# Performance work log

Measured on AMD Instinct MI355X. Metric: run time of the kernel, lower is better.

Reference implementation:

```python
import jax, jax.numpy as jnp
import numpy as np

LN_EPS = 1e-5
ALPHA_Q = 1.0

def _ln(t, g, b):
    mu = jnp.mean(t, -1, keepdims=True)
    var = jnp.var(t, -1, keepdims=True)
    return (t - mu) / jnp.sqrt(var + LN_EPS) * g + b

def _mlp(t, w1, b1, w2, b2):
    h = jax.nn.gelu(t @ w1.T + b1, approximate=False)
    return h @ w2.T + b2

def setup_inputs() -> dict:
    key = jax.random.key(0)
    B, N, L, E, H, D = 2, 2048, 2048, 1024, 16, 4
    ks = jax.random.split(key, 40)
    rn = lambda i, shape, sc: jax.random.normal(ks[i], shape, jnp.float32) * sc
    inp = {}
    inp['x'] = rn(0, (B, N, E), 1.0)
    inp['xp'] = jax.random.uniform(ks[1], (B, N, D), jnp.float32)
    inp['y'] = rn(2, (B, L, E), 1.0)
    inp['yp'] = jax.random.uniform(ks[3], (B, L, D), jnp.float32)
    inp['attn_mask'] = jax.random.uniform(ks[4], (1, 1, N, L), jnp.float32)
    # PositionEncoder params (torch Linear convention: weight [out,in])
    inp['p_w1'] = rn(5, (E, D), 1.0 / D)
    inp['p_b1'] = jax.random.uniform(ks[6], (E,), jnp.float32, 0.0, np.pi)
    inp['p_w2'] = rn(7, (E, D), 1.0 / D)
    inp['p_b2'] = jax.random.uniform(ks[8], (E,), jnp.float32, 0.0, np.pi)
    # QueryEncoder: LayerNorm + mlp1 + mlp2 (mlp0 is dead code in the source)
    inp['q_ln_g'] = jnp.ones((E,), jnp.float32); inp['q_ln_b'] = jnp.zeros((E,), jnp.float32)
    inp['q_m1_w1'] = rn(9, (2 * E, E), 0.02); inp['q_m1_b1'] = jnp.zeros((2 * E,), jnp.float32)
    inp['q_m1_w2'] = rn(10, (E, 2 * E), 0.02); inp['q_m1_b2'] = jnp.zeros((E,), jnp.float32)
    inp['q_m2_w1'] = rn(11, (2 * E, E), 0.02); inp['q_m2_b1'] = jnp.zeros((2 * E,), jnp.float32)
    inp['q_m2_w2'] = rn(12, (E, 2 * E), 0.02); inp['q_m2_b2'] = jnp.zeros((E,), jnp.float32)
    # KeyEncoder: LayerNorm + mlp1 (mlp0 dead code)
    inp['k_ln_g'] = jnp.ones((E,), jnp.float32); inp['k_ln_b'] = jnp.zeros((E,), jnp.float32)
    inp['k_m1_w1'] = rn(13, (2 * E, E), 0.02); inp['k_m1_b1'] = jnp.zeros((2 * E,), jnp.float32)
    inp['k_m1_w2'] = rn(14, (E, 2 * E), 0.02); inp['k_m1_b2'] = jnp.zeros((E,), jnp.float32)
    # V: LayerNorm + Linear
    inp['v_ln_g'] = jnp.ones((E,), jnp.float32); inp['v_ln_b'] = jnp.zeros((E,), jnp.float32)
    inp['v_w'] = rn(15, (E, E), 0.02); inp['v_b'] = jnp.zeros((E,), jnp.float32)
    # output projections
    inp['proj1_w'] = rn(16, (E, E), 0.02); inp['proj1_b'] = jnp.zeros((E,), jnp.float32)
    inp['proj2_w'] = rn(17, (E, D * H), 0.02); inp['proj2_b'] = jnp.zeros((E,), jnp.float32)
    return inp

def reference(x, xp, y, yp, attn_mask, p_w1, p_b1, p_w2, p_b2,
              q_ln_g, q_ln_b, q_m1_w1, q_m1_b1, q_m1_w2, q_m1_b2,
              q_m2_w1, q_m2_b1, q_m2_w2, q_m2_b2,
              k_ln_g, k_ln_b, k_m1_w1, k_m1_b1, k_m1_w2, k_m1_b2,
              v_ln_g, v_ln_b, v_w, v_b, proj1_w, proj1_b, proj2_w, proj2_b):
    B, N, E = x.shape
    L = y.shape[1]
    D = xp.shape[2]
    H = proj2_w.shape[1] // D
    C = E // H
    # PositionEncoder: query side with bias, key side without bias
    pxt = ALPHA_Q * xp
    xp1 = pxt @ p_w1.T + p_b1            # [B,N,E]
    xp2 = pxt @ p_w2.T + p_b2
    pyt = ALPHA_Q * yp
    yp1 = pyt @ p_w1.T                   # [B,L,E], no bias
    yp2 = pyt @ p_w2.T
    rh = lambda t: t.reshape(t.shape[0], -1, H, C)
    # QueryEncoder
    xn = _ln(x, q_ln_g, q_ln_b)
    x1 = _mlp(xn, q_m1_w1, q_m1_b1, q_m1_w2, q_m1_b2)
    x2 = _mlp(xn, q_m2_w1, q_m2_b1, q_m2_w2, q_m2_b2)
    q = jnp.concatenate([rh(x1 * jnp.cos(xp1)), rh(x1 * jnp.sin(xp1)),
                         rh(x2 * jnp.cos(xp2)), rh(x2 * jnp.sin(xp2))], axis=-1)  # [B,N,H,4C]
    # KeyEncoder (note: second cos/sin block is the raw position code)
    yn = _ln(y, k_ln_g, k_ln_b)
    y1 = _mlp(yn, k_m1_w1, k_m1_b1, k_m1_w2, k_m1_b2)
    k = jnp.concatenate([rh(y1 * jnp.cos(yp1)), rh(y1 * jnp.sin(yp1)),
                         rh(jnp.cos(yp2)), rh(jnp.sin(yp2))], axis=-1)            # [B,L,H,4C]
    scale = (4 * C) ** (-0.5)
    attn = jax.nn.softmax(jnp.einsum('bnhd,blhd->bhnl', q, k) * scale, axis=-1)
    # masked renormalization (mask applied AFTER softmax)
    eps = min(1e-8, 1.0 / L)
    attn = attn * attn_mask
    attn = attn / (jnp.sum(attn, axis=-1, keepdims=True) + eps)
    # values
    v = (_ln(y, v_ln_g, v_ln_b) @ v_w.T + v_b).reshape(B, L, H, C)
    out1 = jnp.einsum('bhnl,blhc->bnhc', attn, v).reshape(B, N, E) @ proj1_w.T + proj1_b
    out2 = jnp.einsum('bhnl,bld->bnhd', attn, yp) - xp[:, :, None, :]             # [B,N,H,D]
    out2 = out2.reshape(B, N, H * D) @ proj2_w.T + proj2_b
    return (out1 + out2, attn, xp)
```

## Files before the change

kernel.cpp:

```cpp
#include <hip/hip_runtime.h>
#include <math.h>
#include <stdint.h>

#define DEV static __device__ __forceinline__

typedef __bf16 bf16x8 __attribute__((ext_vector_type(8)));
typedef __bf16 bf16x4v __attribute__((ext_vector_type(4)));
typedef float f32x4 __attribute__((ext_vector_type(4)));

constexpr int Nn = 2048, Ll = 2048, Ee = 1024, Hh = 16;
constexpr float SCALE = 0.0625f;

constexpr size_t OFF_XN   = 0;
constexpr size_t OFF_YNK  = 8388608;
constexpr size_t OFF_YNV  = 16777216;
constexpr size_t OFF_H12  = 25165824;
constexpr size_t OFF_H3   = 58720256;
constexpr size_t OFF_X1   = 75497472;
constexpr size_t OFF_X2   = 83886080;
constexpr size_t OFF_Y1   = 92274688;
constexpr size_t OFF_QWS  = 100663296;
constexpr size_t OFF_KWS  = 134217728;
constexpr size_t OFF_VWS  = 167772160;
constexpr size_t OFF_DNV  = 176160768;
constexpr size_t OFF_YPT  = 176422912;
constexpr size_t OFF_MSK  = 176685056;
constexpr size_t OFF_AVZ  = 185073664;
constexpr size_t OFF_W1122= 193986560;
constexpr size_t OFF_W12  = 202375168;
constexpr size_t OFF_W22  = 206569472;
constexpr size_t OFF_WK1  = 210763776;
constexpr size_t OFF_WK2  = 214958080;
constexpr size_t OFF_WV   = 219152384;
constexpr size_t OFF_WP   = 221249536;
constexpr size_t OFF_EM   = 223477760;

DEV void gl2l(const void* g, void* l) {
  __builtin_amdgcn_global_load_lds((const __attribute__((address_space(1))) void*)g,
                                   (__attribute__((address_space(3))) void*)l, 16, 0, 0);
}

DEV float gelu_f(float v) {
  float x = v * 0.70710678118654752f;
  float ax = fabsf(x);
  float t = 1.f / fmaf(0.3275911f, ax, 1.f);
  float y = t * fmaf(t, fmaf(t, fmaf(t, fmaf(t, 1.061405429f, -1.453152027f),
                                     1.421413741f), -0.284496736f), 0.254829592f);
  float er = 1.f - y * __expf(-x * x);
  er = (x < 0.f) ? -er : er;
  return 0.5f * v * (1.f + er);
}

__launch_bounds__(256)
__global__ void prep_ln(const float* __restrict__ s0, const float* __restrict__ s1,
                        const float* __restrict__ s2, const float* __restrict__ s3,
                        const float* __restrict__ s4, const float* __restrict__ s5,
                        const float* __restrict__ s6,
                        __bf16* __restrict__ d0, __bf16* __restrict__ d1,
                        __bf16* __restrict__ d2, __bf16* __restrict__ d3,
                        __bf16* __restrict__ d4, __bf16* __restrict__ d5,
                        __bf16* __restrict__ d6,
                        const float* __restrict__ pw1, const float* __restrict__ pw2,
                        __bf16* __restrict__ wp,
                        const float* __restrict__ mask, __bf16* __restrict__ mb,
                        const float* __restrict__ yp, __bf16* __restrict__ ypT,
                        const float* __restrict__ x, const float* __restrict__ y,
                        const float* __restrict__ qg, const float* __restrict__ qb,
                        const float* __restrict__ kg, const float* __restrict__ kb,
                        const float* __restrict__ vg, const float* __restrict__ vb,
                        __bf16* __restrict__ xn, __bf16* __restrict__ ynk,
                        __bf16* __restrict__ ynv) {
  const int tid = threadIdx.x;
  if (blockIdx.x >= 18512) {
    const int t = blockIdx.x - 18512;
    const bool isx = t < 4096;
    const int row = isx ? t : t - 4096;
    const float* src = (isx ? x : y) + (size_t)row * Ee;
    const float4 v = ((const float4*)src)[tid];
    float s = v.x + v.y + v.z + v.w;
    float q = v.x*v.x + v.y*v.y + v.z*v.z + v.w*v.w;
    #pragma unroll
    for (int o = 32; o > 0; o >>= 1) { s += __shfl_down(s, o); q += __shfl_down(q, o); }
    __shared__ float ls[4], lq[4];
    if ((tid & 63) == 0) { ls[tid >> 6] = s; lq[tid >> 6] = q; }
    __syncthreads();
    s = ls[0] + ls[1] + ls[2] + ls[3];
    q = lq[0] + lq[1] + lq[2] + lq[3];
    const float mu = s * (1.f / Ee);
    const float rstd = rsqrtf(q * (1.f / Ee) - mu * mu + 1e-5f);
    const int e0 = tid << 2;
    float h0 = (v.x - mu) * rstd, h1 = (v.y - mu) * rstd,
          h2 = (v.z - mu) * rstd, h3 = (v.w - mu) * rstd;
    if (isx) {
      bf16x4v o;
      o[0] = (__bf16)(h0 * qg[e0]   + qb[e0]);
      o[1] = (__bf16)(h1 * qg[e0+1] + qb[e0+1]);
      o[2] = (__bf16)(h2 * qg[e0+2] + qb[e0+2]);
      o[3] = (__bf16)(h3 * qg[e0+3] + qb[e0+3]);
      *(bf16x4v*)(xn + (size_t)row * Ee + e0) = o;
    } else {
      bf16x4v ok, ov;
      ok[0] = (__bf16)(h0 * kg[e0]   + kb[e0]);
      ok[1] = (__bf16)(h1 * kg[e0+1] + kb[e0+1]);
      ok[2] = (__bf16)(h2 * kg[e0+2] + kb[e0+2]);
      ok[3] = (__bf16)(h3 * kg[e0+3] + kb[e0+3]);
      ov[0] = (__bf16)(h0 * vg[e0]   + vb[e0]);
      ov[1] = (__bf16)(h1 * vg[e0+1] + vb[e0+1]);
      ov[2] = (__bf16)(h2 * vg[e0+2] + vb[e0+2]);
      ov[3] = (__bf16)(h3 * vg[e0+3] + vb[e0+3]);
      *(bf16x4v*)(ynk + (size_t)row * Ee + e0) = ok;
      *(bf16x4v*)(ynv + (size_t)row * Ee + e0) = ov;
    }
    return;
  }
  int u = blockIdx.x * 256 + tid;
  if (u < 3407872) {
    int seg = u >> 19, r = u & 524287;
    const float* s; __bf16* d;
    if      (seg == 0) { s = s0; d = d0; }
    else if (seg == 1) { s = s1; d = d1; }
    else if (seg == 2) { s = s2; d = d2; }
    else if (seg == 3) { s = s3; d = d3; }
    else if (seg == 4) { s = s4; d = d4; }
    else if (seg == 5) { s = s5; d = d5; }
    else               { s = s6; d = d6; }
    float4 v = ((const float4*)s)[r];
    bf16x4v o; o[0]=(__bf16)v.x; o[1]=(__bf16)v.y; o[2]=(__bf16)v.z; o[3]=(__bf16)v.w;
    ((bf16x4v*)d)[r] = o;
  } else if (u < 3686400) {
    int p = u - 3407872;
    int row = p / 272, c4 = p - row * 272;
    float4 v = (c4 < 256) ? ((const float4*)pw1)[row * 256 + c4]
                          : ((const float4*)pw2)[row * 16 + (c4 - 256)];
    bf16x4v o; o[0]=(__bf16)v.x; o[1]=(__bf16)v.y; o[2]=(__bf16)v.z; o[3]=(__bf16)v.w;
    *(bf16x4v*)(wp + (size_t)row * 1088 + (c4 << 2)) = o;
  } else if (u < 4734976) {
    int q = u - 3686400;
    float4 v = ((const float4*)mask)[q];
    bf16x4v o; o[0]=(__bf16)v.x; o[1]=(__bf16)v.y; o[2]=(__bf16)v.z; o[3]=(__bf16)v.w;
    ((bf16x4v*)mb)[q] = o;
  } else {
    int t0 = (u - 4734976) << 2;
    #pragma unroll
    for (int k = 0; k < 4; k++) {
      int i = t0 + k;
      int b = i >> 13, d = (i >> 11) & 3, l = i & 2047;
      ypT[i] = (__bf16)yp[(((size_t)b << 11) + l) * 4 + d];
    }
  }
}

#define STAGE_A(BM_, A_, lda_, kt_, kh_, buf_)                                        \
  _Pragma("unroll")                                                                   \
  for (int jj = 0; jj < (BM_) / 128; jj++) {                                          \
    int c = (jj << 9) + tid;                                                          \
    int row_ = c >> 2, j_ = c & 3;                                                    \
    int col_ = ((kt_) << 6) + ((kh_) << 5) + ((j_ ^ (row_ & 3)) << 3);                \
    gl2l(A_ + (size_t)(m0 + row_) * (lda_) + col_,                                    \
         As + ((((buf_) << 1) + (kh_)) * ((BM_) * 32)) + (c << 3));                   \
  }

#define STAGE_B(W_, ldw_, kt_, kh_, buf_)                                             \
  _Pragma("unroll")                                                                   \
  for (int jj = 0; jj < 2; jj++) {                                                    \
    int c = (jj << 9) + tid;                                                          \
    int row_ = c >> 2, j_ = c & 3;                                                    \
    int col_ = ((kt_) << 6) + ((kh_) << 5) + ((j_ ^ (row_ & 3)) << 3);                \
    gl2l(W_ + (size_t)(n0 + row_) * (ldw_) + col_,                                    \
         Bs + ((((buf_) << 1) + (kh_)) * 8192) + (c << 3));                           \
  }

#define LOAD_A(BM_, buf_, ks_)                                                        \
  _Pragma("unroll")                                                                   \
  for (int i = 0; i < (BM_) / 32; i++) {                                              \
    int ra = wm + (i << 4) + li;                                                      \
    af[i] = *(const bf16x8*)(As + ((((buf_) << 1) + (ks_)) * ((BM_) * 32))            \
             + ra * 32 + ((g ^ (ra & 3)) << 3));                                      \
  }

#define LOAD_B(buf_, ks_, qn_)                                                        \
  _Pragma("unroll")                                                                   \
  for (int jj = 0; jj < 2; jj++) {                                                    \
    int rb = wn + ((qn_) << 5) + (jj << 4) + li;                                      \
    bw[jj] = *(const bf16x8*)(Bs + ((((buf_) << 1) + (ks_)) * 8192)                   \
             + rb * 32 + ((g ^ (rb & 3)) << 3));                                      \
  }

#define MFMA_Q(BM_, qn_)                                                              \
  __builtin_amdgcn_s_setprio(1);                                                      \
  _Pragma("unroll")                                                                   \
  for (int i = 0; i < (BM_) / 32; i++) {                                              \
    acc[i][((qn_) << 1)]     = __builtin_amdgcn_mfma_f32_16x16x32_bf16(af[i], bw[0], acc[i][((qn_) << 1)], 0, 0, 0);     \
    acc[i][((qn_) << 1) + 1] = __builtin_amdgcn_mfma_f32_16x16x32_bf16(af[i], bw[1], acc[i][((qn_) << 1) + 1], 0, 0, 0); \
  }                                                                                   \
  __builtin_amdgcn_s_setprio(0);

#define PH_SYNC                                                                       \
  __builtin_amdgcn_s_barrier();                                                       \
  asm volatile("s_waitcnt lgkmcnt(0)" ::: "memory");                                  \
  __builtin_amdgcn_sched_barrier(0);

#define PH_END __builtin_amdgcn_s_barrier();

#define GEMM_PIPE(BM_, A_, lda_, W_, ldw_, K_)                                        \
  const int w = tid >> 6, lane = tid & 63, g = lane >> 4, li = lane & 15;             \
  const int wm = (w >> 2) * ((BM_) / 2), wn = (w & 3) << 6;                           \
  constexpr int MI_ = (BM_) / 32;                                                     \
  constexpr int VMC = (BM_) / 128 + 2;                                                \
  f32x4 acc[MI_][4];                                                                  \
  _Pragma("unroll")                                                                   \
  for (int i = 0; i < MI_; i++)                                                       \
    _Pragma("unroll")                                                                 \
    for (int j = 0; j < 4; j++) acc[i][j] = (f32x4)0.f;                               \
  STAGE_A(BM_, A_, lda_, 0, 0, 0) STAGE_B(W_, ldw_, 0, 0, 0)                          \
  STAGE_A(BM_, A_, lda_, 0, 1, 0) STAGE_B(W_, ldw_, 0, 1, 0)                          \
  STAGE_A(BM_, A_, lda_, 1, 0, 1) STAGE_B(W_, ldw_, 1, 0, 1)                          \
  asm volatile("s_waitcnt vmcnt(%0)" :: "i"(VMC) : "memory");                         \
  __builtin_amdgcn_s_barrier();                                                       \
  const int NT = (K_) >> 6;                                                           \
  bf16x8 af[MI_], bw[2];                                                              \
  for (int t = 0; t < NT; t++) {                                                      \
    const int buf = t & 1, nbuf = buf ^ 1;                                            \
    const bool sB = (t + 1 < NT);                                                     \
    const bool sA = (t + 2 < NT);                                                     \
    LOAD_A(BM_, buf, 0) LOAD_B(buf, 0, 0)                                             \
    if (sB) { STAGE_A(BM_, A_, lda_, t + 1, 1, nbuf) }                                \
    PH_SYNC MFMA_Q(BM_, 0) PH_END                                                     \
    LOAD_B(buf, 0, 1)                                                                 \
    if (sB) {                                                                         \
      STAGE_B(W_, ldw_, t + 1, 1, nbuf)                                               \
      asm volatile("s_waitcnt vmcnt(%0)" :: "i"(VMC) : "memory");                     \
    } else {                                                                          \
      asm volatile("s_waitcnt vmcnt(0)" ::: "memory");                                \
    }                                                                                 \
    PH_SYNC MFMA_Q(BM_, 1) PH_END                                                     \
    LOAD_A(BM_, buf, 1) LOAD_B(buf, 1, 0)                                             \
    if (sA) { STAGE_A(BM_, A_, lda_, t + 2, 0, buf) }                                 \
    PH_SYNC MFMA_Q(BM_, 0) PH_END                                                     \
    LOAD_B(buf, 1, 1)                                                                 \
    if (sA) {                                                                         \
      STAGE_B(W_, ldw_, t + 2, 0, buf)                                                \
      asm volatile("s_waitcnt vmcnt(%0)" :: "i"(VMC) : "memory");                     \
    } else if (t + 1 < NT) {                                                          \
      asm volatile("s_waitcnt vmcnt(0)" ::: "memory");                                \
    }                                                                                 \
    PH_SYNC MFMA_Q(BM_, 1) PH_END                                                     \
  }

__launch_bounds__(512, 2)
__global__ void gemm_mlp1(const __bf16* __restrict__ xn, const __bf16* __restrict__ ynk,
                          const __bf16* __restrict__ w1122, const __bf16* __restrict__ wk1,
                          const float* __restrict__ qb1, const float* __restrict__ qb2,
                          const float* __restrict__ kb1,
                          __bf16* __restrict__ h12, __bf16* __restrict__ h3) {
  __shared__ __align__(16) __bf16 As[2 * 2 * 256 * 32];
  __shared__ __align__(16) __bf16 Bs[2 * 2 * 256 * 32];
  const int tid = threadIdx.x, bid = blockIdx.x;
  if (bid < 256) {
    const int m0 = (bid >> 4) << 8, n0 = (bid & 15) << 8;
    GEMM_PIPE(256, xn, 1024, w1122, 1024, 1024)
    #pragma unroll
    for (int j = 0; j < 4; j++) {
      int n = n0 + wn + (j << 4) + li;
      float bias = (n < 2048) ? qb1[n] : qb2[n - 2048];
      #pragma unroll
      for (int i = 0; i < MI_; i++) {
        #pragma unroll
        for (int r = 0; r < 4; r++) {
          int m = m0 + wm + (i << 4) + (g << 2) + r;
          h12[(size_t)m * 4096 + n] = (__bf16)gelu_f(acc[i][j][r] + bias);
        }
      }
    }
  } else {
    const int rr = bid - 256;
    const int m0 = (rr >> 3) << 7, n0 = (rr & 7) << 8;
    GEMM_PIPE(128, ynk, 1024, wk1, 1024, 1024)
    #pragma unroll
    for (int j = 0; j < 4; j++) {
      int n = n0 + wn + (j << 4) + li;
      float bias = kb1[n];
      #pragma unroll
      for (int i = 0; i < MI_; i++) {
        #pragma unroll
        for (int r = 0; r < 4; r++) {
          int m = m0 + wm + (i << 4) + (g << 2) + r;
          h3[(size_t)m * 2048 + n] = (__bf16)gelu_f(acc[i][j][r] + bias);
        }
      }
    }
  }
}

__launch_bounds__(512, 2)
__global__ void gemm_mlp2(const __bf16* __restrict__ h12, const __bf16* __restrict__ h3,
                          const __bf16* __restrict__ ynv,
                          const __bf16* __restrict__ w12, const __bf16* __restrict__ w22,
                          const __bf16* __restrict__ wk2, const __bf16* __restrict__ wv,
                          const float* __restrict__ bx1, const float* __restrict__ bx2,
                          const float* __restrict__ by1, const float* __restrict__ bv,
                          __bf16* __restrict__ x1, __bf16* __restrict__ x2,
                          __bf16* __restrict__ y1, __bf16* __restrict__ vT) {
  __shared__ __align__(16) __bf16 As[2 * 2 * 256 * 32];
  __shared__ __align__(16) __bf16 Bs[2 * 2 * 256 * 32];
  const int tid = threadIdx.x, bid = blockIdx.x;
  const int seg = bid >> 6, rr = bid & 63;
  const int m0 = (rr >> 2) << 8, n0 = (rr & 3) << 8;
  const __bf16* A; const __bf16* W; const float* bias; __bf16* out; int lda, K;
  if      (seg == 0) { A = h12;        lda = 4096; W = w12; bias = bx1; out = x1; K = 2048; }
  else if (seg == 1) { A = h12 + 2048; lda = 4096; W = w22; bias = bx2; out = x2; K = 2048; }
  else if (seg == 2) { A = h3;         lda = 2048; W = wk2; bias = by1; out = y1; K = 2048; }
  else               { A = ynv;        lda = 1024; W = wv;  bias = bv;  out = vT; K = 1024; }
  GEMM_PIPE(256, A, lda, W, K, K)
  #pragma unroll
  for (int j = 0; j < 4; j++) {
    int n = n0 + wn + (j << 4) + li;
    float bs = bias[n];
    #pragma unroll
    for (int i = 0; i < MI_; i++) {
      #pragma unroll
      for (int r = 0; r < 4; r++) {
        int m = m0 + wm + (i << 4) + (g << 2) + r;
        float v = acc[i][j][r] + bs;
        if (seg == 3) {
          int bb = m >> 11, l = m & 2047, hh = n >> 6, cc = n & 63;
          vT[(((size_t)(bb * Hh + hh) * 64 + cc) << 11) + l] = (__bf16)v;
        } else {
          out[(size_t)m * 1024 + n] = (__bf16)v;
        }
      }
    }
  }
}

__launch_bounds__(256)
__global__ void build_qk(const __bf16* __restrict__ x1, const __bf16* __restrict__ x2,
                         const float* __restrict__ xp,
                         const __bf16* __restrict__ y1, const float* __restrict__ yp,
                         const float* __restrict__ pw1, const float* __restrict__ pb1,
                         const float* __restrict__ pw2, const float* __restrict__ pb2,
                         __bf16* __restrict__ q_ws, __bf16* __restrict__ k_ws) {
  const bool isq = blockIdx.x < 2048;
  const int bid = isq ? blockIdx.x : blockIdx.x - 2048;
  const int t = (bid << 1) + (threadIdx.x >> 7);
  const int tl = threadIdx.x & 127;
  const int b = t >> 11, n = t & 2047;
  const int hh = tl >> 3, ch = tl & 7;
  const int e0 = (hh << 6) + (ch << 3);
  const float* pos = isq ? xp : yp;
  const float p0 = pos[(size_t)t*4], p1 = pos[(size_t)t*4+1],
              p2 = pos[(size_t)t*4+2], p3 = pos[(size_t)t*4+3];
  bf16x8 o0, o1, o2, o3;
  if (isq) {
    bf16x8 v1 = *(const bf16x8*)(x1 + (size_t)t * Ee + e0);
    bf16x8 v2 = *(const bf16x8*)(x2 + (size_t)t * Ee + e0);
    #pragma unroll
    for (int sub = 0; sub < 8; sub++) {
      int e = e0 + sub;
      float a1 = pw1[e*4]*p0 + pw1[e*4+1]*p1 + pw1[e*4+2]*p2 + pw1[e*4+3]*p3 + pb1[e];
      float a2 = pw2[e*4]*p0 + pw2[e*4+1]*p1 + pw2[e*4+2]*p2 + pw2[e*4+3]*p3 + pb2[e];
      float s1, c1, s2, c2;
      __sincosf(a1, &s1, &c1); __sincosf(a2, &s2, &c2);
      float xv1 = (float)v1[sub], xv2 = (float)v2[sub];
      o0[sub] = (__bf16)(xv1 * c1); o1[sub] = (__bf16)(xv1 * s1);
      o2[sub] = (__bf16)(xv2 * c2); o3[sub] = (__bf16)(xv2 * s2);
    }
  } else {
    bf16x8 v1 = *(const bf16x8*)(y1 + (size_t)t * Ee + e0);
    #pragma unroll
    for (int sub = 0; sub < 8; sub++) {
      int e = e0 + sub;
      float a1 = pw1[e*4]*p0 + pw1[e*4+1]*p1 + pw1[e*4+2]*p2 + pw1[e*4+3]*p3;
      float a2 = pw2[e*4]*p0 + pw2[e*4+1]*p1 + pw2[e*4+2]*p2 + pw2[e*4+3]*p3;
      float s1, c1, s2, c2;
      __sincosf(a1, &s1, &c1); __sincosf(a2, &s2, &c2);
      float yv = (float)v1[sub];
      o0[sub] = (__bf16)(yv * c1); o1[sub] = (__bf16)(yv * s1);
      o2[sub] = (__bf16)c2;        o3[sub] = (__bf16)s2;
    }
  }
  const int k = n & 7, bc = ch ^ k;
  __bf16* base = (isq ? q_ws : k_ws) + ((((size_t)b * Hh + hh) * Nn + n) << 8);
  *(bf16x8*)(base + ((bc          ) << 3)) = o0;
  *(bf16x8*)(base + (((8  ^ k) ^ ch) << 3)) = o1;
  *(bf16x8*)(base + (((16 ^ k) ^ ch) << 3)) = o2;
  *(bf16x8*)(base + (((24 ^ k) ^ ch) << 3)) = o3;
}

__launch_bounds__(512, 1)
__global__ void attn_fused(const __bf16* __restrict__ q_ws, const __bf16* __restrict__ k_ws,
                           const __bf16* __restrict__ vT_ws, const __bf16* __restrict__ ypT_g,
                           const __bf16* __restrict__ mask_bf, const float* __restrict__ xp,
                           __bf16* __restrict__ em_g, float* __restrict__ dinv_g,
                           __bf16* __restrict__ avz) {
  __shared__ __align__(16) __bf16 kq[2][64 * 256];
  __shared__ __align__(16) __bf16 vt[2][64 * 72];
  __shared__ __align__(16) __bf16 pT[256 * 72];
  __shared__ __align__(16) __bf16 ypl[2][16 * 72];
  __shared__ float te_s[256];
  const int tid = threadIdx.x, w = tid >> 6, lane = tid & 63, g = lane >> 4, li = lane & 15;
  const int logical = ((blockIdx.x & 7) << 5) + (blockIdx.x >> 3);
  const int bh = logical >> 3, nt = logical & 7;
  const int b = bh >> 4, h = bh & 15;
  const int n0 = nt << 8;
  const __bf16* qb = q_ws + (((size_t)bh * Nn + n0) << 8);
  const __bf16* kb = k_ws + (((size_t)bh * Ll) << 8);
  const __bf16* vb = vT_ws + ((size_t)bh << 17);
  const __bf16* yb = ypT_g + ((size_t)b << 13);
  const __bf16* mb = mask_bf + ((size_t)n0 << 11);

  bf16x8 aq[2][8];
  #pragma unroll
  for (int rf = 0; rf < 2; rf++) {
    const int nloc = (w << 5) + (rf << 4) + li;
    #pragma unroll
    for (int s = 0; s < 8; s++)
      aq[rf][s] = *(const bf16x8*)(qb + ((size_t)nloc << 8) + ((((s << 2) + g) ^ (nloc & 7)) << 3));
  }
  for (int i = tid; i < 1728; i += 512) {
    int buf = i / 864, idx = i - buf * 864;
    ypl[buf][288 + idx] = (__bf16)0.f;
  }
  {
    const int vc = tid >> 3, vl = (tid & 7) << 3;
    bf16x8 vreg = *(const bf16x8*)(vb + ((size_t)vc << 11) + vl);
    bf16x8 ypreg;
    if (tid < 32) ypreg = *(const bf16x8*)(yb + ((size_t)(tid >> 3) << 11) + ((tid & 7) << 3));
    #pragma unroll
    for (int j = 0; j < 4; j++) {
      int c = (j << 9) + tid;
      gl2l(kb + (size_t)(c >> 5) * 256 + ((c & 31) << 3), kq[0] + ((c - lane) << 3));
    }
    *(bf16x8*)(vt[0] + vc * 72 + vl) = vreg;
    if (tid < 32) *(bf16x8*)(ypl[0] + (tid >> 3) * 72 + ((tid & 7) << 3)) = ypreg;
  }
  __syncthreads();

  float se[2][4];
  float te[4] = {0.f, 0.f, 0.f, 0.f};
  f32x4 accv[2][4], accp[2];
  #pragma unroll
  for (int rf = 0; rf < 2; rf++) {
    #pragma unroll
    for (int r = 0; r < 4; r++) se[rf][r] = 0.f;
    #pragma unroll
    for (int cb = 0; cb < 4; cb++) accv[rf][cb] = (f32x4)0.f;
    accp[rf] = (f32x4)0.f;
  }

  for (int t = 0; t < 32; ++t) {
    const int l0 = t << 6, cur = t & 1, nxt = cur ^ 1;
    const bool more = (t < 31);
    bf16x8 mk[4];
    #pragma unroll
    for (int j = 0; j < 4; j++) {
      int q = (j << 6) + lane;
      mk[j] = *(const bf16x8*)(mb + (size_t)((w << 5) + (q >> 3)) * 2048 + l0 + ((q & 7) << 3));
    }
    bf16x8 vreg, ypreg;
    if (more) {
      const int l1 = l0 + 64;
      vreg = *(const bf16x8*)(vb + ((size_t)(tid >> 3) << 11) + l1 + ((tid & 7) << 3));
      if (tid < 32) ypreg = *(const bf16x8*)(yb + ((size_t)(tid >> 3) << 11) + l1 + ((tid & 7) << 3));
      #pragma unroll
      for (int j = 0; j < 4; j++) {
        int c = (j << 9) + tid;
        gl2l(kb + (size_t)(l1 + (c >> 5)) * 256 + ((c & 31) << 3), kq[nxt] + ((c - lane) << 3));
      }
    }
    f32x4 Cs[2][4];
    #pragma unroll
    for (int lb = 0; lb < 4; lb++) { Cs[0][lb] = (f32x4)0.f; Cs[1][lb] = (f32x4)0.f; }
    #pragma unroll
    for (int lb = 0; lb < 4; lb++) {
      const int kr = (lb << 4) + li;
      #pragma unroll
      for (int s = 0; s < 8; s++) {
        bf16x8 bk = *(const bf16x8*)(kq[cur] + kr * 256 + ((((s << 2) + g) ^ (kr & 7)) << 3));
        Cs[0][lb] = __builtin_amdgcn_mfma_f32_16x16x32_bf16(aq[0][s], bk, Cs[0][lb], 0, 0, 0);
        Cs[1][lb] = __builtin_amdgcn_mfma_f32_16x16x32_bf16(aq[1][s], bk, Cs[1][lb], 0, 0, 0);
      }
    }
    #pragma unroll
    for (int rf = 0; rf < 2; rf++) {
      #pragma unroll
      for (int lb = 0; lb < 4; lb++) {
        #pragma unroll
        for (int r = 0; r < 4; r++) {
          const int row = (w << 5) + (rf << 4) + (g << 2) + r;
          float e = __expf(Cs[rf][lb][r] * SCALE);
          se[rf][r] += e;
          pT[row * 72 + (lb << 4) + li] = (__bf16)e;
        }
      }
    }
    asm volatile("s_waitcnt lgkmcnt(0)" ::: "memory");
    __builtin_amdgcn_sched_barrier(0);
    #pragma unroll
    for (int j = 0; j < 4; j++) {
      const int q = (j << 6) + lane;
      const int row = q >> 3, ch = q & 7;
      bf16x8 pv = *(const bf16x8*)(pT + ((w << 5) + row) * 72 + (ch << 3));
      bf16x8 emv;
      float tp = 0.f;
      #pragma unroll
      for (int i = 0; i < 8; i++) {
        float p = (float)pv[i] * (float)mk[j][i];
        emv[i] = (__bf16)p;
        tp += p;
      }
      tp += __shfl_xor(tp, 1);
      tp += __shfl_xor(tp, 2);
      tp += __shfl_xor(tp, 4);
      te[j] += tp;
      *(bf16x8*)(em_g + ((size_t)bh << 22) + ((size_t)(n0 + (w << 5) + row) << 11) + l0 + (ch << 3)) = emv;
      *(bf16x8*)(pT + ((w << 5) + row) * 72 + (ch << 3)) = emv;
    }
    asm volatile("s_waitcnt lgkmcnt(0)" ::: "memory");
    __builtin_amdgcn_sched_barrier(0);
    #pragma unroll
    for (int kc = 0; kc < 2; kc++) {
      bf16x8 vv[4];
      #pragma unroll
      for (int cb = 0; cb < 4; cb++)
        vv[cb] = *(const bf16x8*)(vt[cur] + ((cb << 4) + li) * 72 + (kc << 5) + (g << 3));
      bf16x8 yy = *(const bf16x8*)(ypl[cur] + li * 72 + (kc << 5) + (g << 3));
      #pragma unroll
      for (int rf = 0; rf < 2; rf++) {
        bf16x8 pa = *(const bf16x8*)(pT + ((w << 5) + (rf << 4) + li) * 72 + (kc << 5) + (g << 3));
        #pragma unroll
        for (int cb = 0; cb < 4; cb++)
          accv[rf][cb] = __builtin_amdgcn_mfma_f32_16x16x32_bf16(pa, vv[cb], accv[rf][cb], 0, 0, 0);
        accp[rf] = __builtin_amdgcn_mfma_f32_16x16x32_bf16(pa, yy, accp[rf], 0, 0, 0);
      }
    }
    if (more) {
      *(bf16x8*)(vt[nxt] + (tid >> 3) * 72 + ((tid & 7) << 3)) = vreg;
      if (tid < 32) *(bf16x8*)(ypl[nxt] + (tid >> 3) * 72 + ((tid & 7) << 3)) = ypreg;
    }
    __syncthreads();
  }

  if ((lane & 7) == 0) {
    #pragma unroll
    for (int j = 0; j < 4; j++)
      te_s[(w << 5) + (j << 3) + (lane >> 3)] = te[j];
  }
  asm volatile("s_waitcnt lgkmcnt(0)" ::: "memory");
  __builtin_amdgcn_sched_barrier(0);
  __syncthreads();

  #pragma unroll
  for (int rf = 0; rf < 2; rf++) {
    #pragma unroll
    for (int r = 0; r < 4; r++) {
      float s = se[rf][r];
      #pragma unroll
      for (int o = 1; o < 16; o <<= 1) s += __shfl_xor(s, o);
      float tt = te_s[(w << 5) + (rf << 4) + (g << 2) + r];
      float dinv = 1.f / (tt + 1e-8f * s);
      const int n = n0 + (w << 5) + (rf << 4) + (g << 2) + r;
      if (li == 0) dinv_g[((size_t)bh << 11) + n] = dinv;
      #pragma unroll
      for (int cb = 0; cb < 4; cb++)
        avz[((size_t)b * Nn + n) * 1088 + (h << 6) + (cb << 4) + li] = (__bf16)(accv[rf][cb][r] * dinv);
      if (li < 4) {
        float z = accp[rf][r] * dinv - xp[(((size_t)b * Nn + n) << 2) + li];
        avz[((size_t)b * Nn + n) * 1088 + 1024 + (h << 2) + li] = (__bf16)z;
      }
    }
  }
}

__launch_bounds__(256)
__global__ void fin_proj(const __bf16* __restrict__ A, const __bf16* __restrict__ W,
                         const float* __restrict__ bias1, const float* __restrict__ bias2,
                         float* __restrict__ out,
                         const __bf16* __restrict__ em_g, const float* __restrict__ dinv_g,
                         float* __restrict__ attn_out,
                         const float* __restrict__ xp, float* __restrict__ xp_out) {
  constexpr int N = 1024, K = 1088;
  __shared__ __align__(16) __bf16 As[2][128 * 32];
  __shared__ __align__(16) __bf16 Bs[2][64 * 32];
  const int tid = threadIdx.x;
  if (blockIdx.x >= 512) {
    const int sbid = blockIdx.x - 512;
    if (sbid < 64) {
      int idx = sbid * 256 + tid;
      ((float4*)xp_out)[idx] = ((const float4*)xp)[idx];
    }
    for (size_t i8 = sbid * 256ul + tid; i8 < 16777216ul; i8 += 524288ul) {
      bf16x8 v = ((const bf16x8*)em_g)[i8];
      float dv = dinv_g[i8 >> 8];
      float4 o0, o1;
      o0.x = (float)v[0] * dv; o0.y = (float)v[1] * dv; o0.z = (float)v[2] * dv; o0.w = (float)v[3] * dv;
      o1.x = (float)v[4] * dv; o1.y = (float)v[5] * dv; o1.z = (float)v[6] * dv; o1.w = (float)v[7] * dv;
      ((float4*)attn_out)[i8 * 2]     = o0;
      ((float4*)attn_out)[i8 * 2 + 1] = o1;
    }
    return;
  }
  const int w = tid >> 6, lane = tid & 63, g = lane >> 4, li = lane & 15;
  const int bt = blockIdx.x >> 4;
  const int m0 = bt << 7, n0 = (blockIdx.x & 15) << 6;
  const int wm = (w >> 1) << 6, wn = (w & 1) << 5;
  f32x4 acc[4][2];
  #pragma unroll
  for (int i = 0; i < 4; i++) { acc[i][0] = (f32x4)0.f; acc[i][1] = (f32x4)0.f; }
  auto stage = [&](int buf, int kt) {
    const int col0 = kt << 5;
    #pragma unroll
    for (int j = 0; j < 2; j++) {
      int c = (j << 8) + tid;
      int row = c >> 2, sl = c & 3;
      int col = col0 + ((sl ^ (row & 3)) << 3);
      gl2l(A + (size_t)(m0 + row) * K + col, As[buf] + ((c - lane) << 3));
    }
    {
      int c = tid;
      int row = c >> 2, sl = c & 3;
      int col = col0 + ((sl ^ (row & 3)) << 3);
      gl2l(W + (size_t)(n0 + row) * K + col, Bs[buf] + ((c - lane) << 3));
    }
  };
  const int NT = K >> 5;
  stage(0, 0);
  for (int kt = 0; kt < NT; kt++) {
    const int cur = kt & 1;
    if (kt + 1 < NT) {
      stage(cur ^ 1, kt + 1);
      asm volatile("s_waitcnt vmcnt(3)" ::: "memory");
    } else {
      asm volatile("s_waitcnt vmcnt(0)" ::: "memory");
    }
    __builtin_amdgcn_s_barrier();
    __builtin_amdgcn_sched_barrier(0);
    bf16x8 af[4], bw[2];
    #pragma unroll
    for (int i = 0; i < 4; i++) {
      int ra = wm + (i << 4) + li;
      af[i] = *(const bf16x8*)(As[cur] + ra * 32 + ((g ^ (ra & 3)) << 3));
    }
    #pragma unroll
    for (int j = 0; j < 2; j++) {
      int rb = wn + (j << 4) + li;
      bw[j] = *(const bf16x8*)(Bs[cur] + rb * 32 + ((g ^ (rb & 3)) << 3));
    }
    #pragma unroll
    for (int i = 0; i < 4; i++)
      #pragma unroll
      for (int j = 0; j < 2; j++)
        acc[i][j] = __builtin_amdgcn_mfma_f32_16x16x32_bf16(af[i], bw[j], acc[i][j], 0, 0, 0);
    asm volatile("s_waitcnt lgkmcnt(0)" ::: "memory");
    __builtin_amdgcn_sched_barrier(0);
    __builtin_amdgcn_s_barrier();
  }
  #pragma unroll
  for (int j = 0; j < 2; j++) {
    int n = n0 + wn + (j << 4) + li;
    float bias = bias1[n] + bias2[n];
    #pragma unroll
    for (int i = 0; i < 4; i++) {
      #pragma unroll
      for (int r = 0; r < 4; r++) {
        int m = m0 + wm + (i << 4) + (g << 2) + r;
        out[(size_t)m * N + n] = acc[i][j][r] + bias;
      }
    }
  }
}

extern "C" void kernel_launch(void* const* d_in, const int* in_sizes, int n_in,
                              void* d_out, int out_size, void* d_ws, size_t ws_size,
                              hipStream_t stream) {
  (void)in_sizes; (void)n_in; (void)out_size; (void)ws_size;
  const float* x       = (const float*)d_in[0];
  const float* xp      = (const float*)d_in[1];
  const float* y       = (const float*)d_in[2];
  const float* yp      = (const float*)d_in[3];
  const float* mask    = (const float*)d_in[4];
  const float* p_w1    = (const float*)d_in[5];
  const float* p_b1    = (const float*)d_in[6];
  const float* p_w2    = (const float*)d_in[7];
  const float* p_b2    = (const float*)d_in[8];
  const float* q_ln_g  = (const float*)d_in[9];
  const float* q_ln_b  = (const float*)d_in[10];
  const float* q_m1_w1 = (const float*)d_in[11];
  const float* q_m1_b1 = (const float*)d_in[12];
  const float* q_m1_w2 = (const float*)d_in[13];
  const float* q_m1_b2 = (const float*)d_in[14];
  const float* q_m2_w1 = (const float*)d_in[15];
  const float* q_m2_b1 = (const float*)d_in[16];
  const float* q_m2_w2 = (const float*)d_in[17];
  const float* q_m2_b2 = (const float*)d_in[18];
  const float* k_ln_g  = (const float*)d_in[19];
  const float* k_ln_b  = (const float*)d_in[20];
  const float* k_m1_w1 = (const float*)d_in[21];
  const float* k_m1_b1 = (const float*)d_in[22];
  const float* k_m1_w2 = (const float*)d_in[23];
  const float* k_m1_b2 = (const float*)d_in[24];
  const float* v_ln_g  = (const float*)d_in[25];
  const float* v_ln_b  = (const float*)d_in[26];
  const float* v_w     = (const float*)d_in[27];
  const float* v_b     = (const float*)d_in[28];
  const float* proj1_w = (const float*)d_in[29];
  const float* proj1_b = (const float*)d_in[30];
  const float* proj2_w = (const float*)d_in[31];
  const float* proj2_b = (const float*)d_in[32];

  char* ws = (char*)d_ws;
  __bf16* xn    = (__bf16*)(ws + OFF_XN);
  __bf16* ynk   = (__bf16*)(ws + OFF_YNK);
  __bf16* ynv   = (__bf16*)(ws + OFF_YNV);
  __bf16* h12   = (__bf16*)(ws + OFF_H12);
  __bf16* h3    = (__bf16*)(ws + OFF_H3);
  __bf16* x1    = (__bf16*)(ws + OFF_X1);
  __bf16* x2    = (__bf16*)(ws + OFF_X2);
  __bf16* y1    = (__bf16*)(ws + OFF_Y1);
  __bf16* q_ws  = (__bf16*)(ws + OFF_QWS);
  __bf16* k_ws  = (__bf16*)(ws + OFF_KWS);
  __bf16* vT_ws = (__bf16*)(ws + OFF_VWS);
  float*  dinv  = (float*)(ws + OFF_DNV);
  __bf16* ypT   = (__bf16*)(ws + OFF_YPT);
  __bf16* mskb  = (__bf16*)(ws + OFF_MSK);
  __bf16* avz   = (__bf16*)(ws + OFF_AVZ);
  __bf16* w1122 = (__bf16*)(ws + OFF_W1122);
  __bf16* w12   = (__bf16*)(ws + OFF_W12);
  __bf16* w22   = (__bf16*)(ws + OFF_W22);
  __bf16* wk1   = (__bf16*)(ws + OFF_WK1);
  __bf16* wk2   = (__bf16*)(ws + OFF_WK2);
  __bf16* wv    = (__bf16*)(ws + OFF_WV);
  __bf16* wp    = (__bf16*)(ws + OFF_WP);
  __bf16* em    = (__bf16*)(ws + OFF_EM);

  float* out0     = (float*)d_out;
  float* attn_out = out0 + (size_t)4194304;
  float* xp_out   = out0 + (size_t)138412032;

  prep_ln<<<26704, 256, 0, stream>>>(q_m1_w1, q_m2_w1, q_m1_w2, q_m2_w2, k_m1_w1, k_m1_w2, v_w,
                                     w1122, w1122 + 2097152, w12, w22, wk1, wk2, wv,
                                     proj1_w, proj2_w, wp, mask, mskb, yp, ypT,
                                     x, y, q_ln_g, q_ln_b, k_ln_g, k_ln_b, v_ln_g, v_ln_b,
                                     xn, ynk, ynv);
  gemm_mlp1<<<512, 512, 0, stream>>>(xn, ynk, w1122, wk1, q_m1_b1, q_m2_b1, k_m1_b1, h12, h3);
  gemm_mlp2<<<256, 512, 0, stream>>>(h12, h3, ynv, w12, w22, wk2, wv,
                                     q_m1_b2, q_m2_b2, k_m1_b2, v_b, x1, x2, y1, vT_ws);
  build_qk<<<4096, 256, 0, stream>>>(x1, x2, xp, y1, yp, p_w1, p_b1, p_w2, p_b2, q_ws, k_ws);
  attn_fused<<<256, 512, 0, stream>>>(q_ws, k_ws, vT_ws, ypT, mskb, xp, em, dinv, avz);
  fin_proj<<<2560, 256, 0, stream>>>(avz, wp, proj1_b, proj2_b, out0,
                                     em, dinv, attn_out, xp, xp_out);
}
```

Measured before the change: 623.2 us.

## Move attention-matrix normalization and xp copy into attention kernel epilogue

The final scaling of the bf16 unnormalized attention matrix by the per-row inverse denominator, and the xp copy, move out of the projection kernel's extra blocks and into the tail of attn_fused. Each attention block rescales and writes its own 256 rows of the fp32 attention output, so the projection GEMM shrinks to a pure 512-block launch. The em data was just written by the same block and may still be in cache. In exchange, this streaming tail now runs on only 256 blocks at one block per CU, with no overlap with the projection GEMM, which may underuse memory bandwidth.

```diff
diff --git a/kernel.cpp b/kernel.cpp
--- a/kernel.cpp
+++ b/kernel.cpp
@@ -392,7 +392,8 @@
                            const __bf16* __restrict__ vT_ws, const __bf16* __restrict__ ypT_g,
                            const __bf16* __restrict__ mask_bf, const float* __restrict__ xp,
                            __bf16* __restrict__ em_g, float* __restrict__ dinv_g,
-                           __bf16* __restrict__ avz) {
+                           __bf16* __restrict__ avz, float* __restrict__ attn_out,
+                           float* __restrict__ xp_out) {
   __shared__ __align__(16) __bf16 kq[2][64 * 256];
   __shared__ __align__(16) __bf16 vt[2][64 * 72];
   __shared__ __align__(16) __bf16 pT[256 * 72];
@@ -409,6 +410,11 @@
   const __bf16* yb = ypT_g + ((size_t)b << 13);
   const __bf16* mb = mask_bf + ((size_t)n0 << 11);
 
+  {
+    int idx = (blockIdx.x << 6) + (tid & 63);
+    if (tid < 64) ((float4*)xp_out)[idx] = ((const float4*)xp)[idx];
+  }
+
   bf16x8 aq[2][8];
   #pragma unroll
   for (int rf = 0; rf < 2; rf++) {
@@ -560,7 +566,10 @@
       float tt = te_s[(w << 5) + (rf << 4) + (g << 2) + r];
       float dinv = 1.f / (tt + 1e-8f * s);
       const int n = n0 + (w << 5) + (rf << 4) + (g << 2) + r;
-      if (li == 0) dinv_g[((size_t)bh << 11) + n] = dinv;
+      if (li == 0) {
+        dinv_g[((size_t)bh << 11) + n] = dinv;
+        te_s[(w << 5) + (rf << 4) + (g << 2) + r] = dinv;
+      }
       #pragma unroll
       for (int cb = 0; cb < 4; cb++)
         avz[((size_t)b * Nn + n) * 1088 + (h << 6) + (cb << 4) + li] = (__bf16)(accv[rf][cb][r] * dinv);
@@ -570,36 +579,32 @@
       }
     }
   }
+  __syncthreads();
+
+  const __bf16* em_base = em_g + ((size_t)bh << 22) + ((size_t)n0 << 11);
+  float* ao_base = attn_out + ((size_t)bh << 22) + ((size_t)n0 << 11);
+  for (int p = 0; p < 128; p++) {
+    int c = (p << 9) + tid;
+    int row = c >> 8, ch = c & 255;
+    bf16x8 v = *(const bf16x8*)(em_base + ((size_t)row << 11) + (ch << 3));
+    float dv = te_s[row];
+    float4 o0, o1;
+    o0.x = (float)v[0] * dv; o0.y = (float)v[1] * dv; o0.z = (float)v[2] * dv; o0.w = (float)v[3] * dv;
+    o1.x = (float)v[4] * dv; o1.y = (float)v[5] * dv; o1.z = (float)v[6] * dv; o1.w = (float)v[7] * dv;
+    float* dst = ao_base + ((size_t)row << 11) + (ch << 3);
+    *(float4*)dst = o0;
+    *(float4*)(dst + 4) = o1;
+  }
 }
 
 __launch_bounds__(256)
-__global__ void fin_proj(const __bf16* __restrict__ A, const __bf16* __restrict__ W,
-                         const float* __restrict__ bias1, const float* __restrict__ bias2,
-                         float* __restrict__ out,
-                         const __bf16* __restrict__ em_g, const float* __restrict__ dinv_g,
-                         float* __restrict__ attn_out,
-                         const float* __restrict__ xp, float* __restrict__ xp_out) {
+__global__ void gemm_proj(const __bf16* __restrict__ A, const __bf16* __restrict__ W,
+                          const float* __restrict__ bias1, const float* __restrict__ bias2,
+                          float* __restrict__ out) {
   constexpr int N = 1024, K = 1088;
   __shared__ __align__(16) __bf16 As[2][128 * 32];
   __shared__ __align__(16) __bf16 Bs[2][64 * 32];
   const int tid = threadIdx.x;
-  if (blockIdx.x >= 512) {
-    const int sbid = blockIdx.x - 512;
-    if (sbid < 64) {
-      int idx = sbid * 256 + tid;
-      ((float4*)xp_out)[idx] = ((const float4*)xp)[idx];
-    }
-    for (size_t i8 = sbid * 256ul + tid; i8 < 16777216ul; i8 += 524288ul) {
-      bf16x8 v = ((const bf16x8*)em_g)[i8];
-      float dv = dinv_g[i8 >> 8];
-      float4 o0, o1;
-      o0.x = (float)v[0] * dv; o0.y = (float)v[1] * dv; o0.z = (float)v[2] * dv; o0.w = (float)v[3] * dv;
-      o1.x = (float)v[4] * dv; o1.y = (float)v[5] * dv; o1.z = (float)v[6] * dv; o1.w = (float)v[7] * dv;
-      ((float4*)attn_out)[i8 * 2]     = o0;
-      ((float4*)attn_out)[i8 * 2 + 1] = o1;
-    }
-    return;
-  }
   const int w = tid >> 6, lane = tid & 63, g = lane >> 4, li = lane & 15;
   const int bt = blockIdx.x >> 4;
   const int m0 = bt << 7, n0 = (blockIdx.x & 15) << 6;
@@ -746,7 +751,7 @@
   gemm_mlp2<<<256, 512, 0, stream>>>(h12, h3, ynv, w12, w22, wk2, wv,
                                      q_m1_b2, q_m2_b2, k_m1_b2, v_b, x1, x2, y1, vT_ws);
   build_qk<<<4096, 256, 0, stream>>>(x1, x2, xp, y1, yp, p_w1, p_b1, p_w2, p_b2, q_ws, k_ws);
-  attn_fused<<<256, 512, 0, stream>>>(q_ws, k_ws, vT_ws, ypT, mskb, xp, em, dinv, avz);
-  fin_proj<<<2560, 256, 0, stream>>>(avz, wp, proj1_b, proj2_b, out0,
-                                     em, dinv, attn_out, xp, xp_out);
-}
+  attn_fused<<<256, 512, 0, stream>>>(q_ws, k_ws, vT_ws, ypT, mskb, xp, em, dinv, avz,
+                                      attn_out, xp_out);
+  gemm_proj<<<512, 256, 0, stream>>>(avz, wp, proj1_b, proj2_b, out0);
+}
```

After: 593.8 us, median of 4. -4.7%, faster.
